# Performance work log

Hardware: AMD Instinct MI355X
Metric: run time of the kernel (lower is better)

## Reference

```python
import jax, jax.numpy as jnp
import numpy as np

BATCH = 8192
K_DIM = 4096   # input_dim
N_DIM = 4096   # output_dim
MEM = 1048576  # size of shared hashed weight vector
SEED = 1367
BLOCK = 32     # RzLinear tile size (BLOCK_K = BLOCK_N = 32)
_P = np.int64(2147483647)  # large prime used for tile hashing


def _weight_indices(H, K, N, seed, block):
    """Static int32 index map [K, N] -> hashed_weight, mimicking RzLinear's
    per-tile hash: each (block x block) tile of W is a contiguous row-major
    chunk of hashed_weight starting at ((kb*R3 + nb*R2 + R1) % P) % (H - block*block)."""
    rng = np.random.RandomState(seed)
    R1, R2, R3 = rng.randint(1, 2**31 - 1, size=3).astype(np.int64)
    kb, nb = K // block, N // block
    kk = np.arange(kb, dtype=np.int64)[:, None]
    nn = np.arange(nb, dtype=np.int64)[None, :]
    start = ((kk * R3 + nn * R2 + R1) % _P) % np.int64(H - block * block)  # [kb, nb]
    local = (np.arange(block, dtype=np.int64)[:, None] * block
             + np.arange(block, dtype=np.int64)[None, :])                  # [block, block]
    idx = start[:, :, None, None] + local[None, None, :, :]                # [kb, nb, block, block]
    idx = idx.transpose(0, 2, 1, 3).reshape(K, N)
    return jnp.asarray(idx, dtype=jnp.int32)


_IDX = _weight_indices(MEM, K_DIM, N_DIM, SEED, BLOCK)


def setup_inputs() -> dict:
    key = jax.random.key(0)
    k1, k2 = jax.random.split(key)
    x = jax.random.normal(k1, (BATCH, K_DIM), dtype=jnp.float32)
    # scale like a fan-in init so outputs/norms stay O(1)
    hashed_weight = jax.random.normal(k2, (MEM,), dtype=jnp.float32) / np.float32(np.sqrt(K_DIM))
    return {"x": x, "hashed_weight": hashed_weight}


def reference(x, hashed_weight):
    # Irregular gather: reconstruct effective weight [K, N] from shared vector
    W = hashed_weight[_IDX]
    y = x @ W                                   # [B, N]
    # torch.norm(y, dim=1).view(-1, 1)
    return jnp.linalg.norm(y, axis=1, keepdims=True)  # [B, 1]
```

## Files before the change

### kernel.cpp

```cpp
#include <hip/hip_runtime.h>
#include <stdint.h>
#include <math.h>

typedef __bf16 bf16;
typedef float f32x4 __attribute__((ext_vector_type(4)));
typedef int   i32x4 __attribute__((ext_vector_type(4)));

#define B_DIM 8192
#define K_DIM 4096
#define N_DIM 4096
#define MEM_H 1048576
#define HMOD  1047552
#define NT    (K_DIM / 64)

static void mt_randint3(uint32_t seed, long long R[3]) {
  uint32_t mt[624];
  mt[0] = seed;
  for (int i = 1; i < 624; i++)
    mt[i] = 1812433253u * (mt[i - 1] ^ (mt[i - 1] >> 30)) + (uint32_t)i;
  int pos = 624;
  auto next32 = [&]() -> uint32_t {
    if (pos >= 624) {
      for (int i = 0; i < 624; i++) {
        uint32_t y = (mt[i] & 0x80000000u) | (mt[(i + 1) % 624] & 0x7fffffffu);
        uint32_t v = mt[(i + 397) % 624] ^ (y >> 1);
        if (y & 1u) v ^= 0x9908b0dfu;
        mt[i] = v;
      }
      pos = 0;
    }
    uint32_t y = mt[pos++];
    y ^= y >> 11;
    y ^= (y << 7) & 0x9d2c5680u;
    y ^= (y << 15) & 0xefc60000u;
    y ^= y >> 18;
    return y;
  };
  for (int j = 0; j < 3; j++) {
    uint32_t v;
    do { v = next32() & 0x7fffffffu; } while (v > 0x7ffffffdu);
    R[j] = 1LL + (long long)v;
  }
}

__device__ __forceinline__ uint32_t q8(float v) {
  int q = (int)rintf(v * 32.0f);
  q = q > 127 ? 127 : (q < -127 ? -127 : q);
  return (uint32_t)(q & 0xFF);
}

__global__ void k_prep(const float* __restrict__ x, uint8_t* __restrict__ xq,
                       const float* __restrict__ hw, uint8_t* __restrict__ wq,
                       long long R1, long long R2, long long R3) {
  if (blockIdx.x < 8192) {
    int id = blockIdx.x * 256 + threadIdx.x;
    const float* base = x + (size_t)id * 16;
    uint32_t r[4];
#pragma unroll
    for (int j = 0; j < 4; j++) {
      f32x4 v = *(const f32x4*)(base + j * 4);
      r[j] = q8(v[0]) | (q8(v[1]) << 8) | (q8(v[2]) << 16) | (q8(v[3]) << 24);
    }
    ((uint4*)xq)[id] = make_uint4(r[0], r[1], r[2], r[3]);
  } else {
    int tile = blockIdx.x - 8192;
    int kb = tile & 127, nb = tile >> 7;
    long long v = (long long)kb * R3 + (long long)nb * R2 + R1;
    int start = (int)((v % 2147483647LL) % (long long)HMOD);
    const float* src = hw + start;
    int t = threadIdx.x;
    int nl = t >> 3, k4 = t & 7;
    uint32_t b = 0;
#pragma unroll
    for (int j = 0; j < 4; j++)
      b |= q8(src[(k4 * 4 + j) * 32 + nl] * 64.0f) << (8 * j);
    *(uint32_t*)(wq + (size_t)(nb * 32 + nl) * 4096 + kb * 32 + k4 * 4) = b;
  }
}

__device__ __forceinline__ void gload_lds16(const void* g, void* l) {
  __builtin_amdgcn_global_load_lds(
      (const __attribute__((address_space(1))) void*)g,
      (__attribute__((address_space(3))) void*)l, 16, 0, 0);
}

#define SGB() __builtin_amdgcn_sched_barrier(0)
#define VMC(n)  do { SGB(); asm volatile("s_waitcnt vmcnt(" #n ")"); SGB(); } while (0)
#define LGKM(n) do { SGB(); asm volatile("s_waitcnt lgkmcnt(" #n ")"); SGB(); } while (0)
#define BAR() __builtin_amdgcn_s_barrier()
#define DSR128(dst, base, off) \
  asm volatile("ds_read_b128 %0, %1 offset:" off : "=&v"(dst) : "v"(base))

#define FM(RH, R4, CB, AF)                                                     \
  acc[(RH)*4 + (R4)][CB] = __builtin_amdgcn_mfma_i32_16x16x64_i8(              \
      AF[R4], bg[CB], acc[(RH)*4 + (R4)][CB], 0, 0, 0)
#define FM4(RH, CB, AF) do {                                                   \
  FM(RH, 0, CB, AF); FM(RH, 1, CB, AF);                                        \
  FM(RH, 2, CB, AF); FM(RH, 3, CB, AF); } while (0)

__global__ __launch_bounds__(512, 2) void k_gemm(const uint8_t* __restrict__ Aq,
                                                 const uint8_t* __restrict__ Bq,
                                                 float* __restrict__ partial) {
  __shared__ uint8_t smq[2][2][2][128 * 64];
  int bid = blockIdx.x;
  int swz = (bid & 7) * 64 + (bid >> 3);
  int mt = swz & 31, nt = swz >> 5;
  int tid = threadIdx.x;
  int w = tid >> 6, lane = tid & 63;
  int wm = w >> 2, wn = w & 3;
  int lr = lane & 15, lk = lane >> 4;
  size_t bm = (size_t)mt * 256, bn = (size_t)nt * 256;
  const uint8_t* Ab = Aq + (bm << 12);
  const uint8_t* Bb = Bq + (bn << 12);

  i32x4 acc[8][4] = {};
  i32x4 afE[4], afO[4], bg[4];

  auto STAGE_A = [&](int h, int tt, int buf) {
    gload_lds16(Ab + ((size_t)(h * 128 + w * 16 + lr) << 12) + tt * 64 + lk * 16,
                &smq[buf][0][h][w * 1024]);
  };
  auto STAGE_B = [&](int h, int tt, int buf) {
    gload_lds16(Bb + ((size_t)(h * 128 + w * 16 + lr) << 12) + tt * 64 + lk * 16,
                &smq[buf][1][h][w * 1024]);
  };

  uint32_t smb = (uint32_t)(uintptr_t)
      (__attribute__((address_space(3))) uint8_t*)&smq[0][0][0][0];
  uint32_t aA = smb + wm * 8192 + lane * 16;
  uint32_t aB = smb + 16384 + (wn >> 1) * 8192 + (wn & 1) * 4096 + lane * 16;

  STAGE_A(0, 0, 0); STAGE_A(1, 0, 0);
  STAGE_B(0, 0, 0); STAGE_B(1, 0, 0);
  STAGE_A(0, 1, 1); STAGE_A(1, 1, 1);
  STAGE_B(0, 1, 1); STAGE_B(1, 1, 1);
  VMC(4);
  BAR();
  DSR128(afE[0], aA, "0");    DSR128(afE[1], aA, "1024");
  DSR128(afE[2], aA, "2048"); DSR128(afE[3], aA, "3072");
  DSR128(bg[0], aB, "0");     DSR128(bg[1], aB, "1024");

  for (int t = 0; t < NT; t++) {
    int t2 = (t + 2 < NT) ? t + 2 : NT - 1;
    int cur = t & 1;
    uint32_t bsel = (uint32_t)cur << 15;
    uint32_t Ac = aA + bsel, Bc = aB + bsel;
    uint32_t An = Ac ^ 32768u, Bn = Bc ^ 32768u;

    LGKM(0);
    __builtin_amdgcn_s_setprio(1);
    FM4(0, 0, afE);
    SGB();
    DSR128(bg[2], Bc, "2048"); DSR128(bg[3], Bc, "3072");
    SGB();
    FM4(0, 1, afE);
    __builtin_amdgcn_s_setprio(0);

    LGKM(0);
    __builtin_amdgcn_s_setprio(1);
    FM(0, 0, 2, afE); FM(0, 0, 3, afE);
    SGB();
    DSR128(afO[0], Ac, "4096"); DSR128(afO[1], Ac, "5120");
    DSR128(afO[2], Ac, "6144"); DSR128(afO[3], Ac, "7168");
    SGB();
    FM(0, 1, 2, afE); FM(0, 2, 2, afE); FM(0, 3, 2, afE);
    FM(0, 1, 3, afE); FM(0, 2, 3, afE); FM(0, 3, 3, afE);
    __builtin_amdgcn_s_setprio(0);
    BAR();

    LGKM(0);
    __builtin_amdgcn_s_setprio(1);
    FM4(1, 0, afO); FM4(1, 1, afO);
    __builtin_amdgcn_s_setprio(0);
    STAGE_B(0, t2, cur); STAGE_B(1, t2, cur);
    VMC(2);
    BAR();

    __builtin_amdgcn_s_setprio(1);
    FM(1, 0, 2, afO); FM(1, 0, 3, afO);
    SGB();
    DSR128(afE[0], An, "0");    DSR128(afE[1], An, "1024");
    DSR128(afE[2], An, "2048"); DSR128(afE[3], An, "3072");
    DSR128(bg[0], Bn, "0");     DSR128(bg[1], Bn, "1024");
    SGB();
    FM(1, 1, 2, afO); FM(1, 2, 2, afO); FM(1, 3, 2, afO);
    FM(1, 1, 3, afO); FM(1, 2, 3, afO); FM(1, 3, 3, afO);
    __builtin_amdgcn_s_setprio(0);
    STAGE_A(0, t2, cur); STAGE_A(1, t2, cur);
  }
  VMC(0);
  LGKM(0);

#pragma unroll
  for (int rb = 0; rb < 8; rb++) {
#pragma unroll
    for (int reg = 0; reg < 4; reg++) {
      float s = 0.f;
#pragma unroll
      for (int cb = 0; cb < 4; cb++) {
        float v = (float)acc[rb][cb][reg];
        s += v * v;
      }
      s += __shfl_xor(s, 1);
      s += __shfl_xor(s, 2);
      s += __shfl_xor(s, 4);
      s += __shfl_xor(s, 8);
      if (lr == 0) {
        int row = (int)bm + wm * 128 + rb * 16 + lk * 4 + reg;
        partial[(size_t)(nt * 4 + wn) * B_DIM + row] = s;
      }
    }
  }
}

__global__ void k_finish(const float* __restrict__ partial, float* __restrict__ out) {
  int b = blockIdx.x * 256 + threadIdx.x;
  float s = 0.f;
#pragma unroll
  for (int i = 0; i < 64; i++) s += partial[(size_t)i * B_DIM + b];
  out[b] = sqrtf(s) * (1.0f / 65536.0f);
}

extern "C" void kernel_launch(void* const* d_in, const int* in_sizes, int n_in,
                              void* d_out, int out_size, void* d_ws, size_t ws_size,
                              hipStream_t stream) {
  const float* x  = (const float*)d_in[0];
  const float* hw = (const float*)d_in[1];
  float* out = (float*)d_out;
  char* ws = (char*)d_ws;
  uint8_t* xq = (uint8_t*)ws;
  uint8_t* wq = (uint8_t*)(ws + (size_t)B_DIM * K_DIM);
  float* partial = (float*)(ws + (size_t)B_DIM * K_DIM
                               + (size_t)K_DIM * N_DIM);
  long long R[3];
  mt_randint3(1367u, R);

  k_prep<<<8192 + 16384, 256, 0, stream>>>(x, xq, hw, wq, R[0], R[1], R[2]);
  k_gemm<<<(B_DIM / 256) * (N_DIM / 256), 512, 0, stream>>>(xq, wq, partial);
  k_finish<<<B_DIM / 256, 256, 0, stream>>>(partial, out);
}
```

Before: 204.8 us.

## Load B fragments directly from global in MFMA-ready layout, bypassing LDS

The prep kernel now writes quantized weights in a fragment-major layout matching the MFMA B operand, so each lane reads one 16-byte fragment directly. The GEMM then loads B straight from global memory into registers, double-buffered across tiles, instead of staging it through LDS. This halves LDS usage and LDS read traffic and removes a barrier phase. The cost is that B reads now go through global memory and cache without reuse across waves sharing the same columns, plus extra register pressure from the second B buffer.

Result: faster. 185.1 us (-9.6%).

```diff
diff --git a/kernel.cpp b/kernel.cpp
--- a/kernel.cpp
+++ b/kernel.cpp
@@ -74,7 +74,10 @@
 #pragma unroll
     for (int j = 0; j < 4; j++)
       b |= q8(src[(k4 * 4 + j) * 32 + nl] * 64.0f) << (8 * j);
-    *(uint32_t*)(wq + (size_t)(nb * 32 + nl) * 4096 + kb * 32 + k4 * 4) = b;
+    int n = nb * 32 + nl;
+    int frag = (n >> 4) * 64 + (kb >> 1);
+    int lane16 = (n & 15) + ((kb & 1) * 2 + (k4 >> 2)) * 16;
+    *(uint32_t*)(wq + (size_t)frag * 1024 + lane16 * 16 + (k4 & 3) * 4) = b;
   }
 }
 
@@ -90,18 +93,59 @@
 #define BAR() __builtin_amdgcn_s_barrier()
 #define DSR128(dst, base, off) \
   asm volatile("ds_read_b128 %0, %1 offset:" off : "=&v"(dst) : "v"(base))
-
-#define FM(RH, R4, CB, AF)                                                     \
+#define GLB128(dst, ptr) \
+  asm volatile("global_load_dwordx4 %0, %1, off" : "=&v"(dst) : "v"(ptr))
+
+#define FM(RH, R4, CB, AF, BG)                                                 \
   acc[(RH)*4 + (R4)][CB] = __builtin_amdgcn_mfma_i32_16x16x64_i8(              \
-      AF[R4], bg[CB], acc[(RH)*4 + (R4)][CB], 0, 0, 0)
-#define FM4(RH, CB, AF) do {                                                   \
-  FM(RH, 0, CB, AF); FM(RH, 1, CB, AF);                                        \
-  FM(RH, 2, CB, AF); FM(RH, 3, CB, AF); } while (0)
+      AF[R4], BG[CB], acc[(RH)*4 + (R4)][CB], 0, 0, 0)
+#define FM8(RH, C0, C1, AF, BG) do {                                           \
+  FM(RH, 0, C0, AF, BG); FM(RH, 1, C0, AF, BG);                                \
+  FM(RH, 2, C0, AF, BG); FM(RH, 3, C0, AF, BG);                                \
+  FM(RH, 0, C1, AF, BG); FM(RH, 1, C1, AF, BG);                                \
+  FM(RH, 2, C1, AF, BG); FM(RH, 3, C1, AF, BG); } while (0)
+
+#define TILE(T, BGC, BGN) do {                                                 \
+  int t1c = ((T) + 1 < NT) ? (T) + 1 : NT - 1;                                 \
+  int t2c = ((T) + 2 < NT) ? (T) + 2 : NT - 1;                                 \
+  int cur = (T) & 1;                                                           \
+  uint32_t bsel = (uint32_t)cur << 14;                                         \
+  uint32_t Ac = aA + bsel, An = aA + (16384u - bsel);                          \
+                    \
+  LGKM(0);                                                                     \
+  __builtin_amdgcn_s_setprio(1);                                               \
+  FM8(0, 0, 1, afE, BGC);                                                      \
+  SGB();                                                                       \
+  DSR128(afO[0], Ac, "4096"); DSR128(afO[1], Ac, "5120");                      \
+  DSR128(afO[2], Ac, "6144"); DSR128(afO[3], Ac, "7168");                      \
+  GLB128(BGN[0], Bw + t1c * 1024);                                             \
+  GLB128(BGN[1], Bw + 65536 + t1c * 1024);                                     \
+  GLB128(BGN[2], Bw + 131072 + t1c * 1024);                                    \
+  GLB128(BGN[3], Bw + 196608 + t1c * 1024);                                    \
+  SGB();                                                                       \
+  FM8(0, 2, 3, afE, BGC);                                                      \
+  __builtin_amdgcn_s_setprio(0);                                               \
+     \
+  LGKM(0);                                                                     \
+  BAR();                                                                       \
+  STAGE_A(0, t2c, cur); STAGE_A(1, t2c, cur);                                  \
+  VMC(6);                                                                      \
+  BAR();                                                                       \
+  __builtin_amdgcn_s_setprio(1);                                               \
+  FM8(1, 0, 1, afO, BGC);                                                      \
+  SGB();                                                                       \
+  DSR128(afE[0], An, "0");    DSR128(afE[1], An, "1024");                      \
+  DSR128(afE[2], An, "2048"); DSR128(afE[3], An, "3072");                      \
+  SGB();                                                                       \
+  FM8(1, 2, 3, afO, BGC);                                                      \
+  __builtin_amdgcn_s_setprio(0);                                               \
+  VMC(2);                                                                      \
+} while (0)
 
 __global__ __launch_bounds__(512, 2) void k_gemm(const uint8_t* __restrict__ Aq,
                                                  const uint8_t* __restrict__ Bq,
                                                  float* __restrict__ partial) {
-  __shared__ uint8_t smq[2][2][2][128 * 64];
+  __shared__ uint8_t smq[2][16384];
   int bid = blockIdx.x;
   int swz = (bid & 7) * 64 + (bid >> 3);
   int mt = swz & 31, nt = swz >> 5;
@@ -109,84 +153,36 @@
   int w = tid >> 6, lane = tid & 63;
   int wm = w >> 2, wn = w & 3;
   int lr = lane & 15, lk = lane >> 4;
-  size_t bm = (size_t)mt * 256, bn = (size_t)nt * 256;
+  size_t bm = (size_t)mt * 256;
   const uint8_t* Ab = Aq + (bm << 12);
-  const uint8_t* Bb = Bq + (bn << 12);
+  const uint8_t* Bw = Bq + ((size_t)(nt * 16 + wn * 4) << 16) + lane * 16;
 
   i32x4 acc[8][4] = {};
-  i32x4 afE[4], afO[4], bg[4];
+  i32x4 afE[4], afO[4], bgA[4], bgB[4];
 
   auto STAGE_A = [&](int h, int tt, int buf) {
     gload_lds16(Ab + ((size_t)(h * 128 + w * 16 + lr) << 12) + tt * 64 + lk * 16,
-                &smq[buf][0][h][w * 1024]);
+                &smq[buf][(h * 8 + w) * 1024]);
   };
-  auto STAGE_B = [&](int h, int tt, int buf) {
-    gload_lds16(Bb + ((size_t)(h * 128 + w * 16 + lr) << 12) + tt * 64 + lk * 16,
-                &smq[buf][1][h][w * 1024]);
-  };
 
   uint32_t smb = (uint32_t)(uintptr_t)
-      (__attribute__((address_space(3))) uint8_t*)&smq[0][0][0][0];
+      (__attribute__((address_space(3))) uint8_t*)&smq[0][0];
   uint32_t aA = smb + wm * 8192 + lane * 16;
-  uint32_t aB = smb + 16384 + (wn >> 1) * 8192 + (wn & 1) * 4096 + lane * 16;
-
+
+  GLB128(bgA[0], Bw);
+  GLB128(bgA[1], Bw + 65536);
+  GLB128(bgA[2], Bw + 131072);
+  GLB128(bgA[3], Bw + 196608);
   STAGE_A(0, 0, 0); STAGE_A(1, 0, 0);
-  STAGE_B(0, 0, 0); STAGE_B(1, 0, 0);
   STAGE_A(0, 1, 1); STAGE_A(1, 1, 1);
-  STAGE_B(0, 1, 1); STAGE_B(1, 1, 1);
-  VMC(4);
+  VMC(2);
   BAR();
   DSR128(afE[0], aA, "0");    DSR128(afE[1], aA, "1024");
   DSR128(afE[2], aA, "2048"); DSR128(afE[3], aA, "3072");
-  DSR128(bg[0], aB, "0");     DSR128(bg[1], aB, "1024");
-
-  for (int t = 0; t < NT; t++) {
-    int t2 = (t + 2 < NT) ? t + 2 : NT - 1;
-    int cur = t & 1;
-    uint32_t bsel = (uint32_t)cur << 15;
-    uint32_t Ac = aA + bsel, Bc = aB + bsel;
-    uint32_t An = Ac ^ 32768u, Bn = Bc ^ 32768u;
-
-    LGKM(0);
-    __builtin_amdgcn_s_setprio(1);
-    FM4(0, 0, afE);
-    SGB();
-    DSR128(bg[2], Bc, "2048"); DSR128(bg[3], Bc, "3072");
-    SGB();
-    FM4(0, 1, afE);
-    __builtin_amdgcn_s_setprio(0);
-
-    LGKM(0);
-    __builtin_amdgcn_s_setprio(1);
-    FM(0, 0, 2, afE); FM(0, 0, 3, afE);
-    SGB();
-    DSR128(afO[0], Ac, "4096"); DSR128(afO[1], Ac, "5120");
-    DSR128(afO[2], Ac, "6144"); DSR128(afO[3], Ac, "7168");
-    SGB();
-    FM(0, 1, 2, afE); FM(0, 2, 2, afE); FM(0, 3, 2, afE);
-    FM(0, 1, 3, afE); FM(0, 2, 3, afE); FM(0, 3, 3, afE);
-    __builtin_amdgcn_s_setprio(0);
-    BAR();
-
-    LGKM(0);
-    __builtin_amdgcn_s_setprio(1);
-    FM4(1, 0, afO); FM4(1, 1, afO);
-    __builtin_amdgcn_s_setprio(0);
-    STAGE_B(0, t2, cur); STAGE_B(1, t2, cur);
-    VMC(2);
-    BAR();
-
-    __builtin_amdgcn_s_setprio(1);
-    FM(1, 0, 2, afO); FM(1, 0, 3, afO);
-    SGB();
-    DSR128(afE[0], An, "0");    DSR128(afE[1], An, "1024");
-    DSR128(afE[2], An, "2048"); DSR128(afE[3], An, "3072");
-    DSR128(bg[0], Bn, "0");     DSR128(bg[1], Bn, "1024");
-    SGB();
-    FM(1, 1, 2, afO); FM(1, 2, 2, afO); FM(1, 3, 2, afO);
-    FM(1, 1, 3, afO); FM(1, 2, 3, afO); FM(1, 3, 3, afO);
-    __builtin_amdgcn_s_setprio(0);
-    STAGE_A(0, t2, cur); STAGE_A(1, t2, cur);
+
+  for (int tp = 0; tp < NT / 2; tp++) {
+    TILE(2 * tp, bgA, bgB);
+    TILE(2 * tp + 1, bgB, bgA);
   }
   VMC(0);
   LGKM(0);
```
